# Kernel optimization log

Hardware: AMD Instinct MI355X
Metric: run time of the kernel (lower is better)

The kernel has to match this reference:

```python
import jax, jax.numpy as jnp
import numpy as np

N_NODES = 50000
N_EDGES = 500000
N_GRAPHS = 64
IN_DIM = 6
FFM_DIM = 128
GNN_DIM = 1024
OUT_DIM = 256
SCALES = (1.0, 5.0, 10.0, 30.0)
EPS = 1e-5


def setup_inputs() -> dict:
    key = jax.random.key(0)
    ks = jax.random.split(key, 16)
    x = jax.random.normal(ks[0], (N_NODES, IN_DIM), dtype=jnp.float32)
    edge_index = jax.random.randint(ks[1], (2, N_EDGES), 0, N_NODES, dtype=jnp.int32)
    node_coords = jax.random.normal(ks[2], (N_NODES, 3), dtype=jnp.float32)
    batch = jnp.sort(jax.random.randint(ks[3], (N_NODES,), 0, N_GRAPHS, dtype=jnp.int32))
    s6 = 1.0 / np.sqrt(IN_DIM)
    sg = 1.0 / np.sqrt(GNN_DIM)
    cat_dim = GNN_DIM + len(SCALES) * 2 * FFM_DIM
    sc = 1.0 / np.sqrt(cat_dim)
    return {
        "x": x, "edge_index": edge_index, "node_coords": node_coords, "batch": batch,
        "B": jax.random.normal(ks[4], (3, FFM_DIM), dtype=jnp.float32),
        "W1_l": jax.random.uniform(ks[5], (IN_DIM, GNN_DIM), jnp.float32, -s6, s6),
        "b1": jnp.zeros((GNN_DIM,), jnp.float32),
        "W1_r": jax.random.uniform(ks[6], (IN_DIM, GNN_DIM), jnp.float32, -s6, s6),
        "g1": jnp.ones((GNN_DIM,), jnp.float32), "be1": jnp.zeros((GNN_DIM,), jnp.float32),
        "W2_l": jax.random.uniform(ks[7], (GNN_DIM, GNN_DIM), jnp.float32, -sg, sg),
        "b2": jnp.zeros((GNN_DIM,), jnp.float32),
        "W2_r": jax.random.uniform(ks[8], (GNN_DIM, GNN_DIM), jnp.float32, -sg, sg),
        "g2": jnp.ones((GNN_DIM,), jnp.float32), "be2": jnp.zeros((GNN_DIM,), jnp.float32),
        "Wfc": jax.random.uniform(ks[9], (cat_dim, OUT_DIM), jnp.float32, -sc, sc),
        "bfc": jnp.zeros((OUT_DIM,), jnp.float32),
        "gfc": jnp.ones((OUT_DIM,), jnp.float32), "befc": jnp.zeros((OUT_DIM,), jnp.float32),
    }


def layer_norm(h, g, b):
    mu = jnp.mean(h, axis=-1, keepdims=True)
    var = jnp.mean(jnp.square(h - mu), axis=-1, keepdims=True)
    return (h - mu) * jax.lax.rsqrt(var + EPS) * g + b


def sage_conv(h, src, dst, Wl, bl, Wr):
    # mean aggregation of source features at destination nodes (PyG SAGEConv)
    agg = jax.ops.segment_sum(h[src], dst, num_segments=N_NODES)
    cnt = jax.ops.segment_sum(jnp.ones((src.shape[0],), h.dtype), dst, num_segments=N_NODES)
    agg = agg / jnp.maximum(cnt, 1.0)[:, None]
    return agg @ Wl + bl + h @ Wr


def reference(x, edge_index, node_coords, batch, B, W1_l, b1, W1_r, g1, be1,
              W2_l, b2, W2_r, g2, be2, Wfc, bfc, gfc, befc):
    src, dst = edge_index[0], edge_index[1]
    h = jax.nn.relu(layer_norm(sage_conv(x, src, dst, W1_l, b1, W1_r), g1, be1))
    h = jax.nn.relu(layer_norm(sage_conv(h, src, dst, W2_l, b2, W2_r), g2, be2))
    # multi-scale Fourier features on coordinates
    feats = []
    for s in SCALES:
        proj = (node_coords * s) @ B
        feats.append(jnp.sin(proj))
        feats.append(jnp.cos(proj))
    h_cat = jnp.concatenate([h] + feats, axis=1)
    # global mean pool per graph
    sums = jax.ops.segment_sum(h_cat, batch, num_segments=N_GRAPHS)
    cnts = jax.ops.segment_sum(jnp.ones((N_NODES,), h_cat.dtype), batch, num_segments=N_GRAPHS)
    h_g = sums / jnp.maximum(cnts, 1.0)[:, None]
    return layer_norm(h_g @ Wfc + bfc, gfc, befc)
```

## Files before the change

kernel.cpp:

```cpp
#include <hip/hip_runtime.h>
#include <hip/hip_bf16.h>


#define N_NODES 50000
#define N_EDGES 500000
#define N_GRAPHS 64
#define IN_DIM 6
#define GNN_DIM 1024
#define OUT_DIM 256
#define CAT_DIM 2048
#define M_PAD 50176

typedef __attribute__((ext_vector_type(8))) short short8;
typedef __attribute__((ext_vector_type(4))) float f32x4;

__device__ int g_cnt[N_NODES + 1];
__device__ int g_cursor[N_NODES];
__device__ int g_gcnt[N_GRAPHS];
__device__ int g_rowptr[N_NODES + 1];
__device__ int g_goff[N_GRAPHS + 1];
__device__ int g_esrc[N_EDGES];
__device__ __attribute__((aligned(256))) unsigned short g_w2lt[(size_t)GNN_DIM * GNN_DIM];
__device__ __attribute__((aligned(256))) unsigned short g_w2rt[(size_t)GNN_DIM * GNN_DIM];
__device__ float g_agg1[(size_t)N_NODES * IN_DIM];
__device__ __attribute__((aligned(256))) unsigned short g_h[(size_t)M_PAD * GNN_DIM];
__device__ __attribute__((aligned(256))) unsigned short g_agg2[(size_t)M_PAD * GNN_DIM];
__device__ __attribute__((aligned(256))) unsigned short g_h2[(size_t)M_PAD * GNN_DIM];
__device__ float g_gpool[(size_t)N_GRAPHS * CAT_DIM];

__device__ __forceinline__ float bflo(int u) { return __uint_as_float(((unsigned)u) << 16); }
__device__ __forceinline__ float bfhi(int u) { return __uint_as_float(((unsigned)u) & 0xffff0000u); }
__device__ __forceinline__ unsigned short f2bf(float f) {
    unsigned u = __float_as_uint(f);
    unsigned rounded = u + 0x7fff + ((u >> 16) & 1);
    return (unsigned short)(rounded >> 16);
}
__device__ __forceinline__ int pack2(unsigned short a, unsigned short b) {
    return (int)((unsigned)a | ((unsigned)b << 16));
}

__global__ void zero_kernel() {
    int i = blockIdx.x * 256 + threadIdx.x;
    if (i <= N_NODES) g_cnt[i] = 0;
    if (i < N_NODES) g_cursor[i] = 0;
    if (i < N_GRAPHS) g_gcnt[i] = 0;
    if (i < N_GRAPHS * CAT_DIM) g_gpool[i] = 0.f;
}

__global__ void count_kernel(const int* __restrict__ dst, const int* __restrict__ batch) {
    int i = blockIdx.x * 256 + threadIdx.x;
    if (i < N_EDGES) atomicAdd(&g_cnt[dst[i]], 1);
    if (i < N_NODES) atomicAdd(&g_gcnt[batch[i]], 1);
}

__global__ __launch_bounds__(1024) void scan_kernel() {
    const int CH = 49;
    int t = threadIdx.x;
    int base = t * CH;
    int s = 0;
    #pragma unroll
    for (int i = 0; i < CH; ++i) {
        int n = base + i;
        s += (n < N_NODES) ? g_cnt[n] : 0;
    }
    int lane = t & 63, w = t >> 6;
    int x = s;
    #pragma unroll
    for (int off = 1; off < 64; off <<= 1) {
        int y = __shfl_up(x, off);
        if (lane >= off) x += y;
    }
    __shared__ int wsum[16], woff[16];
    if (lane == 63) wsum[w] = x;
    __syncthreads();
    if (t == 0) { int a = 0; for (int i = 0; i < 16; ++i) { woff[i] = a; a += wsum[i]; } }
    __syncthreads();
    int excl = x - s + woff[w];
    #pragma unroll
    for (int i = 0; i < CH; ++i) {
        int n = base + i;
        if (n <= N_NODES) g_rowptr[n] = excl;
        if (n < N_NODES) excl += g_cnt[n];
    }
    if (t < 64) {
        int v = g_gcnt[t];
        int xx = v;
        #pragma unroll
        for (int off = 1; off < 64; off <<= 1) {
            int y = __shfl_up(xx, off);
            if ((t & 63) >= off) xx += y;
        }
        g_goff[t + 1] = xx;
        if (t == 0) g_goff[0] = 0;
    }
}

__global__ void scatter_kernel(const int* __restrict__ src, const int* __restrict__ dst) {
    int e = blockIdx.x * 256 + threadIdx.x;
    if (e >= N_EDGES) return;
    int d = dst[e];
    int pos = atomicAdd(&g_cursor[d], 1);
    g_esrc[g_rowptr[d] + pos] = src[e];
}

__global__ void transpose_bf16(const float* __restrict__ WA, const float* __restrict__ WB,
                               unsigned short* __restrict__ TA, unsigned short* __restrict__ TB) {
    __shared__ float tile[32][33];
    int id = blockIdx.x & 1023;
    const float* W = (blockIdx.x >> 10) ? WB : WA;
    unsigned short* Wt = (blockIdx.x >> 10) ? TB : TA;
    int bx = id & 31, by = id >> 5;
    int tx = threadIdx.x & 31, ty = threadIdx.x >> 5;
    for (int i = 0; i < 32; i += 8)
        tile[ty + i][tx] = W[(size_t)(by * 32 + ty + i) * GNN_DIM + bx * 32 + tx];
    __syncthreads();
    for (int i = 0; i < 32; i += 8)
        Wt[(size_t)(bx * 32 + ty + i) * GNN_DIM + by * 32 + tx] = f2bf(tile[tx][ty + i]);
}

__global__ void l1_agg_kernel(const float* __restrict__ x) {
    int id = blockIdx.x * 256 + threadIdx.x;
    int n = id >> 3, slot = id & 7;
    if (n >= N_NODES || slot >= IN_DIM) return;
    int beg = g_rowptr[n], end = g_rowptr[n + 1];
    float s = 0.f;
    for (int i = beg; i < end; ++i) s += x[(size_t)g_esrc[i] * IN_DIM + slot];
    g_agg1[n * IN_DIM + slot] = s / (float)max(end - beg, 1);
}

__global__ __launch_bounds__(256) void l1_transform_kernel(
        const float* __restrict__ x,
        const float* __restrict__ W1l, const float* __restrict__ b1,
        const float* __restrict__ W1r, const float* __restrict__ g1,
        const float* __restrict__ be1) {
    int t = threadIdx.x;
    int nb = blockIdx.x * 8;
    float4 wl[6], wr[6];
    #pragma unroll
    for (int k = 0; k < 6; ++k) {
        wl[k] = *(const float4*)&W1l[k * GNN_DIM + t * 4];
        wr[k] = *(const float4*)&W1r[k * GNN_DIM + t * 4];
    }
    float4 bb = *(const float4*)&b1[t * 4];
    float4 gg = *(const float4*)&g1[t * 4];
    float4 be = *(const float4*)&be1[t * 4];
    __shared__ float sx[48], sa[48];
    if (t < 48) sx[t] = x[nb * 6 + t];
    else if (t < 96) sa[t - 48] = g_agg1[nb * 6 + (t - 48)];
    __syncthreads();
    __shared__ float s1[4], s2[4];
    for (int u = 0; u < 8; ++u) {
        int n = nb + u;
        float4 v = bb;
        #pragma unroll
        for (int k = 0; k < 6; ++k) {
            float a = sa[u * 6 + k], xx = sx[u * 6 + k];
            v.x += a * wl[k].x + xx * wr[k].x;
            v.y += a * wl[k].y + xx * wr[k].y;
            v.z += a * wl[k].z + xx * wr[k].z;
            v.w += a * wl[k].w + xx * wr[k].w;
        }
        float sum = v.x + v.y + v.z + v.w;
        float sq  = v.x*v.x + v.y*v.y + v.z*v.z + v.w*v.w;
        #pragma unroll
        for (int off = 32; off; off >>= 1) { sum += __shfl_xor(sum, off); sq += __shfl_xor(sq, off); }
        if ((t & 63) == 0) { s1[t >> 6] = sum; s2[t >> 6] = sq; }
        __syncthreads();
        sum = s1[0] + s1[1] + s1[2] + s1[3];
        sq  = s2[0] + s2[1] + s2[2] + s2[3];
        __syncthreads();
        float mu = sum * (1.f / GNN_DIM);
        float var = sq * (1.f / GNN_DIM) - mu * mu;
        float rstd = rsqrtf(var + 1e-5f);
        float y0 = fmaxf((v.x - mu) * rstd * gg.x + be.x, 0.f);
        float y1 = fmaxf((v.y - mu) * rstd * gg.y + be.y, 0.f);
        float y2 = fmaxf((v.z - mu) * rstd * gg.z + be.z, 0.f);
        float y3 = fmaxf((v.w - mu) * rstd * gg.w + be.w, 0.f);
        int2 pk;
        pk.x = pack2(f2bf(y0), f2bf(y1));
        pk.y = pack2(f2bf(y2), f2bf(y3));
        *(int2*)(g_h + (size_t)n * GNN_DIM + t * 4) = pk;
    }
}

__global__ __launch_bounds__(256) void l2_agg_kernel() {
    int w = threadIdx.x >> 6, lane = threadIdx.x & 63;
    int n = blockIdx.x * 4 + w;
    int beg = g_rowptr[n], end = g_rowptr[n + 1];
    float s[16];
    #pragma unroll
    for (int j = 0; j < 16; ++j) s[j] = 0.f;
    const int4* hp = (const int4*)g_h;
    for (int i = beg; i < end; i += 8) {
        int idx[8]; float msk[8]; int4 va[8], vb[8];
        #pragma unroll
        for (int j = 0; j < 8; ++j) {
            int e = i + j;
            int cl = (e < end) ? e : beg;
            idx[j] = g_esrc[cl];
            msk[j] = (e < end) ? 1.f : 0.f;
        }
        #pragma unroll
        for (int j = 0; j < 8; ++j) {
            va[j] = hp[(size_t)idx[j] * 128 + lane];
            vb[j] = hp[(size_t)idx[j] * 128 + 64 + lane];
        }
        #pragma unroll
        for (int j = 0; j < 8; ++j) {
            float m = msk[j];
            s[0]  += m * bflo(va[j].x); s[1]  += m * bfhi(va[j].x);
            s[2]  += m * bflo(va[j].y); s[3]  += m * bfhi(va[j].y);
            s[4]  += m * bflo(va[j].z); s[5]  += m * bfhi(va[j].z);
            s[6]  += m * bflo(va[j].w); s[7]  += m * bfhi(va[j].w);
            s[8]  += m * bflo(vb[j].x); s[9]  += m * bfhi(vb[j].x);
            s[10] += m * bflo(vb[j].y); s[11] += m * bfhi(vb[j].y);
            s[12] += m * bflo(vb[j].z); s[13] += m * bfhi(vb[j].z);
            s[14] += m * bflo(vb[j].w); s[15] += m * bfhi(vb[j].w);
        }
    }
    float inv = 1.f / (float)max(end - beg, 1);
    int4 o0, o1;
    o0.x = pack2(f2bf(s[0] * inv),  f2bf(s[1] * inv));
    o0.y = pack2(f2bf(s[2] * inv),  f2bf(s[3] * inv));
    o0.z = pack2(f2bf(s[4] * inv),  f2bf(s[5] * inv));
    o0.w = pack2(f2bf(s[6] * inv),  f2bf(s[7] * inv));
    o1.x = pack2(f2bf(s[8] * inv),  f2bf(s[9] * inv));
    o1.y = pack2(f2bf(s[10] * inv), f2bf(s[11] * inv));
    o1.z = pack2(f2bf(s[12] * inv), f2bf(s[13] * inv));
    o1.w = pack2(f2bf(s[14] * inv), f2bf(s[15] * inv));
    *(int4*)(g_agg2 + (size_t)n * GNN_DIM + (size_t)lane * 8) = o0;
    *(int4*)(g_agg2 + (size_t)n * GNN_DIM + 512 + (size_t)lane * 8) = o1;
}

#define BM 128
#define BN 128
#define BK 64

__global__ __launch_bounds__(256) void gemm2_kernel(const float* __restrict__ bias) {
    __shared__ __attribute__((aligned(16))) unsigned short As[BM * BK];
    __shared__ __attribute__((aligned(16))) unsigned short Bs[BN * BK];
    int i = blockIdx.x;
    int xcd = i & 7;
    int j = i >> 3;
    int bm = xcd * 49 + (j >> 3);
    int bn = j & 7;
    int row0 = bm * BM, col0 = bn * BN;
    int t = threadIdx.x;
    int lane = t & 63, wid = t >> 6;
    int wr = wid >> 1, wc = wid & 1;
    f32x4 acc[4][4] = {};
    int c0 = t;
    for (int seg = 0; seg < 2; ++seg) {
        const unsigned short* A  = seg ? g_h : g_agg2;
        const unsigned short* Bt = seg ? g_w2rt : g_w2lt;
        for (int k0 = 0; k0 < GNN_DIM; k0 += BK) {
            __syncthreads();
            #pragma unroll
            for (int u = 0; u < 4; ++u) {
                int c = c0 + u * 256;
                int r = c >> 3;
                int kb = (c & 7) * 16;
                int kbs = kb ^ ((r & 7) << 4);
                __builtin_amdgcn_global_load_lds(
                    (const __attribute__((address_space(1))) void*)(A + (size_t)(row0 + r) * GNN_DIM + k0 + (kbs >> 1)),
                    (__attribute__((address_space(3))) void*)(As + c * 8), 16, 0, 0);
            }
            #pragma unroll
            for (int u = 0; u < 4; ++u) {
                int c = c0 + u * 256;
                int r = c >> 3;
                int kb = (c & 7) * 16;
                int kbs = kb ^ ((r & 7) << 4);
                __builtin_amdgcn_global_load_lds(
                    (const __attribute__((address_space(1))) void*)(Bt + (size_t)(col0 + r) * GNN_DIM + k0 + (kbs >> 1)),
                    (__attribute__((address_space(3))) void*)(Bs + c * 8), 16, 0, 0);
            }
            asm volatile("s_waitcnt vmcnt(0)" ::: "memory");
            __syncthreads();
            #pragma unroll
            for (int kk = 0; kk < BK; kk += 32) {
                short8 a[4], b[4];
                int krd = kk + (lane >> 4) * 8;
                #pragma unroll
                for (int m = 0; m < 4; ++m) {
                    int row = wr * 64 + m * 16 + (lane & 15);
                    int ks = ((krd * 2) ^ ((row & 7) << 4)) >> 1;
                    a[m] = *(const short8*)&As[row * BK + ks];
                }
                #pragma unroll
                for (int n = 0; n < 4; ++n) {
                    int row = wc * 64 + n * 16 + (lane & 15);
                    int ks = ((krd * 2) ^ ((row & 7) << 4)) >> 1;
                    b[n] = *(const short8*)&Bs[row * BK + ks];
                }
                #pragma unroll
                for (int m = 0; m < 4; ++m)
                    #pragma unroll
                    for (int n = 0; n < 4; ++n)
                        acc[m][n] = __builtin_amdgcn_mfma_f32_16x16x32_bf16(a[m], b[n], acc[m][n], 0, 0, 0);
            }
        }
    }
    #pragma unroll
    for (int m = 0; m < 4; ++m) {
        #pragma unroll
        for (int n = 0; n < 4; ++n) {
            int col = col0 + wc * 64 + n * 16 + (lane & 15);
            int rbase = row0 + wr * 64 + m * 16 + (lane >> 4) * 4;
            float bv = bias[col];
            #pragma unroll
            for (int r = 0; r < 4; ++r) {
                float v = acc[m][n][r] + bv;
                g_h2[(size_t)(rbase + r) * GNN_DIM + col] = f2bf(v);
            }
        }
    }
}

__global__ __launch_bounds__(256) void pool_h_kernel(const float* __restrict__ g2,
                                                     const float* __restrict__ be2) {
    int g = blockIdx.x >> 3, sl = blockIdx.x & 7;
    int t = threadIdx.x;
    int beg = g_goff[g], end = g_goff[g + 1];
    int cnt = end - beg;
    int per = (cnt + 7) >> 3;
    int s0 = beg + sl * per, s1v = min(s0 + per, end);
    if (s0 >= s1v) return;
    float4 gg = *(const float4*)&g2[t * 4];
    float4 be = *(const float4*)&be2[t * 4];
    __shared__ float r1[4], r2[4];
    float a0 = 0.f, a1 = 0.f, a2 = 0.f, a3 = 0.f;
    int2 wv = *(const int2*)(g_h2 + (size_t)s0 * GNN_DIM + t * 4);
    for (int n = s0; n < s1v; ++n) {
        int2 w = wv;
        if (n + 1 < s1v) wv = *(const int2*)(g_h2 + (size_t)(n + 1) * GNN_DIM + t * 4);
        float v0 = bflo(w.x), v1 = bfhi(w.x), v2 = bflo(w.y), v3 = bfhi(w.y);
        float sum = v0 + v1 + v2 + v3;
        float sq  = v0*v0 + v1*v1 + v2*v2 + v3*v3;
        #pragma unroll
        for (int off = 32; off; off >>= 1) { sum += __shfl_xor(sum, off); sq += __shfl_xor(sq, off); }
        if ((t & 63) == 0) { r1[t >> 6] = sum; r2[t >> 6] = sq; }
        __syncthreads();
        sum = r1[0] + r1[1] + r1[2] + r1[3];
        sq  = r2[0] + r2[1] + r2[2] + r2[3];
        __syncthreads();
        float mu = sum * (1.f / GNN_DIM);
        float var = sq * (1.f / GNN_DIM) - mu * mu;
        float rstd = rsqrtf(var + 1e-5f);
        a0 += fmaxf((v0 - mu) * rstd * gg.x + be.x, 0.f);
        a1 += fmaxf((v1 - mu) * rstd * gg.y + be.y, 0.f);
        a2 += fmaxf((v2 - mu) * rstd * gg.z + be.z, 0.f);
        a3 += fmaxf((v3 - mu) * rstd * gg.w + be.w, 0.f);
    }
    atomicAdd(&g_gpool[g * CAT_DIM + t * 4 + 0], a0);
    atomicAdd(&g_gpool[g * CAT_DIM + t * 4 + 1], a1);
    atomicAdd(&g_gpool[g * CAT_DIM + t * 4 + 2], a2);
    atomicAdd(&g_gpool[g * CAT_DIM + t * 4 + 3], a3);
}

__global__ __launch_bounds__(256) void pool_f_kernel(const float* __restrict__ coords,
                                                     const float* __restrict__ Bmat) {
    int g = blockIdx.x >> 2, sl = blockIdx.x & 3;
    int t = threadIdx.x;
    int beg = g_goff[g], end = g_goff[g + 1];
    int cnt = end - beg;
    int per = (cnt + 3) >> 2;
    int s0 = beg + sl * per, s1 = min(s0 + per, end);
    const float SC[4] = {1.f, 5.f, 10.f, 30.f};
    int si0 = t >> 7, c0 = t & 127;
    int si1 = si0 + 2;
    float b00 = Bmat[c0] * SC[si0], b01 = Bmat[128 + c0] * SC[si0], b02 = Bmat[256 + c0] * SC[si0];
    float b10 = Bmat[c0] * SC[si1], b11 = Bmat[128 + c0] * SC[si1], b12 = Bmat[256 + c0] * SC[si1];
    float ss0 = 0.f, cs0 = 0.f, ss1 = 0.f, cs1 = 0.f;
    __shared__ float sc[256 * 3];
    for (int base = s0; base < s1; base += 256) {
        int m = min(256, s1 - base);
        __syncthreads();
        for (int q = t; q < 3 * m; q += 256) sc[q] = coords[base * 3 + q];
        __syncthreads();
        for (int i = 0; i < m; ++i) {
            float x0 = sc[i * 3], y0 = sc[i * 3 + 1], z0 = sc[i * 3 + 2];
            float p0 = x0 * b00 + y0 * b01 + z0 * b02;
            float p1 = x0 * b10 + y0 * b11 + z0 * b12;
            ss0 += __sinf(p0); cs0 += __cosf(p0);
            ss1 += __sinf(p1); cs1 += __cosf(p1);
        }
    }
    if (s0 < s1) {
        float* gp = g_gpool + g * CAT_DIM + GNN_DIM;
        atomicAdd(&gp[si0 * 256 + c0], ss0);
        atomicAdd(&gp[si0 * 256 + 128 + c0], cs0);
        atomicAdd(&gp[si1 * 256 + c0], ss1);
        atomicAdd(&gp[si1 * 256 + 128 + c0], cs1);
    }
}

__global__ __launch_bounds__(256) void final_kernel(
        const float* __restrict__ Wfc, const float* __restrict__ bfc,
        const float* __restrict__ gfc, const float* __restrict__ befc,
        float* __restrict__ out) {
    int g = blockIdx.x, t = threadIdx.x;
    int beg = g_goff[g], end = g_goff[g + 1];
    float inv = 1.f / (float)max(end - beg, 1);
    __shared__ float hg[CAT_DIM];
    for (int i = t; i < CAT_DIM; i += 256) hg[i] = g_gpool[g * CAT_DIM + i] * inv;
    __syncthreads();
    float acc = bfc[t];
    for (int k = 0; k < CAT_DIM; ++k) acc = fmaf(hg[k], Wfc[(size_t)k * OUT_DIM + t], acc);
    float sum = acc, sq = acc * acc;
    #pragma unroll
    for (int off = 32; off; off >>= 1) { sum += __shfl_xor(sum, off); sq += __shfl_xor(sq, off); }
    __shared__ float s1[4], s2[4];
    if ((t & 63) == 0) { s1[t >> 6] = sum; s2[t >> 6] = sq; }
    __syncthreads();
    sum = s1[0] + s1[1] + s1[2] + s1[3];
    sq  = s2[0] + s2[1] + s2[2] + s2[3];
    float mu = sum * (1.f / OUT_DIM);
    float var = sq * (1.f / OUT_DIM) - mu * mu;
    float rstd = rsqrtf(var + 1e-5f);
    out[g * OUT_DIM + t] = (acc - mu) * rstd * gfc[t] + befc[t];
}

extern "C" void kernel_launch(void* const* d_in, const int* in_sizes, int n_in,
                              void* d_out, int out_size, void* d_ws, size_t ws_size,
                              hipStream_t stream) {
    const float* x      = (const float*)d_in[0];
    const int*   ei     = (const int*)d_in[1];
    const float* coords = (const float*)d_in[2];
    const int*   batch  = (const int*)d_in[3];
    const float* Bmat   = (const float*)d_in[4];
    const float* W1l    = (const float*)d_in[5];
    const float* b1     = (const float*)d_in[6];
    const float* W1r    = (const float*)d_in[7];
    const float* g1     = (const float*)d_in[8];
    const float* be1    = (const float*)d_in[9];
    const float* W2l    = (const float*)d_in[10];
    const float* b2     = (const float*)d_in[11];
    const float* W2r    = (const float*)d_in[12];
    const float* g2     = (const float*)d_in[13];
    const float* be2    = (const float*)d_in[14];
    const float* Wfc    = (const float*)d_in[15];
    const float* bfc    = (const float*)d_in[16];
    const float* gfc    = (const float*)d_in[17];
    const float* befc   = (const float*)d_in[18];
    const int* src = ei;
    const int* dst = ei + N_EDGES;
    float* out = (float*)d_out;
    (void)in_sizes; (void)n_in; (void)out_size; (void)d_ws; (void)ws_size;

    unsigned short* w2lt;  hipGetSymbolAddress((void**)&w2lt, HIP_SYMBOL(g_w2lt));
    unsigned short* w2rt;  hipGetSymbolAddress((void**)&w2rt, HIP_SYMBOL(g_w2rt));

    zero_kernel<<<512, 256, 0, stream>>>();
    count_kernel<<<(N_EDGES + 255) / 256, 256, 0, stream>>>(dst, batch);
    scan_kernel<<<1, 1024, 0, stream>>>();
    scatter_kernel<<<(N_EDGES + 255) / 256, 256, 0, stream>>>(src, dst);

    transpose_bf16<<<2048, 256, 0, stream>>>(W2l, W2r, w2lt, w2rt);

    l1_agg_kernel<<<(N_NODES * 8 + 255) / 256, 256, 0, stream>>>(x);
    l1_transform_kernel<<<N_NODES / 8, 256, 0, stream>>>(x, W1l, b1, W1r, g1, be1);

    l2_agg_kernel<<<N_NODES / 4, 256, 0, stream>>>();

    gemm2_kernel<<<(M_PAD / BM) * (GNN_DIM / BN), 256, 0, stream>>>(b2);

    pool_h_kernel<<<N_GRAPHS * 8, 256, 0, stream>>>(g2, be2);
    pool_f_kernel<<<N_GRAPHS * 4, 256, 0, stream>>>(coords, Bmat);

    final_kernel<<<N_GRAPHS, 256, 0, stream>>>(Wfc, bfc, gfc, befc, out);
}
```

Baseline: 885.9 us.

## Gather layer-2 neighbor features from an FP8 copy and restructure pooling per wave

```diff
diff --git a/kernel.cpp b/kernel.cpp
--- a/kernel.cpp
+++ b/kernel.cpp
@@ -13,6 +13,12 @@
 
 typedef __attribute__((ext_vector_type(8))) short short8;
 typedef __attribute__((ext_vector_type(4))) float f32x4;
+
+#if defined(__has_builtin)
+#if __has_builtin(__builtin_amdgcn_cvt_pk_fp8_f32) && __has_builtin(__builtin_amdgcn_cvt_pk_f32_fp8)
+#define HW_FP8 1
+#endif
+#endif
 
 __device__ int g_cnt[N_NODES + 1];
 __device__ int g_cursor[N_NODES];
@@ -24,6 +30,7 @@
 __device__ __attribute__((aligned(256))) unsigned short g_w2rt[(size_t)GNN_DIM * GNN_DIM];
 __device__ float g_agg1[(size_t)N_NODES * IN_DIM];
 __device__ __attribute__((aligned(256))) unsigned short g_h[(size_t)M_PAD * GNN_DIM];
+__device__ __attribute__((aligned(256))) unsigned g_h8w[(size_t)M_PAD * (GNN_DIM / 4)];
 __device__ __attribute__((aligned(256))) unsigned short g_agg2[(size_t)M_PAD * GNN_DIM];
 __device__ __attribute__((aligned(256))) unsigned short g_h2[(size_t)M_PAD * GNN_DIM];
 __device__ float g_gpool[(size_t)N_GRAPHS * CAT_DIM];
@@ -38,6 +45,22 @@
 __device__ __forceinline__ int pack2(unsigned short a, unsigned short b) {
     return (int)((unsigned)a | ((unsigned)b << 16));
 }
+
+#ifndef HW_FP8
+__device__ __forceinline__ unsigned enc8(float f) {
+    if (!(f >= 0.015625f)) return 0;
+    if (f > 448.f) f = 448.f;
+    unsigned u = __float_as_uint(f);
+    u += 0x7FFFF + ((u >> 20) & 1);
+    unsigned e = (u >> 23) & 0xFF;
+    return ((e - 120) << 3) | ((u >> 20) & 7);
+}
+__device__ __forceinline__ float dec8(unsigned b) {
+    unsigned e = (b >> 3) & 15, m = b & 7;
+    unsigned f = ((e + 120) << 23) | (m << 20);
+    return e ? __uint_as_float(f) : 0.f;
+}
+#endif
 
 __global__ void zero_kernel() {
     int i = blockIdx.x * 256 + threadIdx.x;
@@ -180,8 +203,28 @@
         pk.x = pack2(f2bf(y0), f2bf(y1));
         pk.y = pack2(f2bf(y2), f2bf(y3));
         *(int2*)(g_h + (size_t)n * GNN_DIM + t * 4) = pk;
-    }
-}
+#ifdef HW_FP8
+        int p8 = __builtin_amdgcn_cvt_pk_fp8_f32(y0, y1, 0, false);
+        p8 = __builtin_amdgcn_cvt_pk_fp8_f32(y2, y3, p8, true);
+        g_h8w[(size_t)n * 256 + t] = (unsigned)p8;
+#else
+        g_h8w[(size_t)n * 256 + t] =
+            enc8(y0) | (enc8(y1) << 8) | (enc8(y2) << 16) | (enc8(y3) << 24);
+#endif
+    }
+}
+
+#ifdef HW_FP8
+#define DEC_ACC(word, b) do { \
+    auto p0_ = __builtin_amdgcn_cvt_pk_f32_fp8((int)(word), false); \
+    auto p1_ = __builtin_amdgcn_cvt_pk_f32_fp8((int)(word), true);  \
+    s[(b)+0] += m * p0_[0]; s[(b)+1] += m * p0_[1]; \
+    s[(b)+2] += m * p1_[0]; s[(b)+3] += m * p1_[1]; } while (0)
+#else
+#define DEC_ACC(word, b) do { unsigned w_ = (unsigned)(word); \
+    s[(b)+0] += m * dec8(w_ & 255);        s[(b)+1] += m * dec8((w_ >> 8) & 255); \
+    s[(b)+2] += m * dec8((w_ >> 16) & 255); s[(b)+3] += m * dec8(w_ >> 24); } while (0)
+#endif
 
 __global__ __launch_bounds__(256) void l2_agg_kernel() {
     int w = threadIdx.x >> 6, lane = threadIdx.x & 63;
@@ -190,9 +233,9 @@
     float s[16];
     #pragma unroll
     for (int j = 0; j < 16; ++j) s[j] = 0.f;
-    const int4* hp = (const int4*)g_h;
+    const int4* hp = (const int4*)g_h8w;
     for (int i = beg; i < end; i += 8) {
-        int idx[8]; float msk[8]; int4 va[8], vb[8];
+        int idx[8]; float msk[8]; int4 v[8];
         #pragma unroll
         for (int j = 0; j < 8; ++j) {
             int e = i + j;
@@ -201,21 +244,12 @@
             msk[j] = (e < end) ? 1.f : 0.f;
         }
         #pragma unroll
-        for (int j = 0; j < 8; ++j) {
-            va[j] = hp[(size_t)idx[j] * 128 + lane];
-            vb[j] = hp[(size_t)idx[j] * 128 + 64 + lane];
-        }
+        for (int j = 0; j < 8; ++j) v[j] = hp[(size_t)idx[j] * 64 + lane];
         #pragma unroll
         for (int j = 0; j < 8; ++j) {
             float m = msk[j];
-            s[0]  += m * bflo(va[j].x); s[1]  += m * bfhi(va[j].x);
-            s[2]  += m * bflo(va[j].y); s[3]  += m * bfhi(va[j].y);
-            s[4]  += m * bflo(va[j].z); s[5]  += m * bfhi(va[j].z);
-            s[6]  += m * bflo(va[j].w); s[7]  += m * bfhi(va[j].w);
-            s[8]  += m * bflo(vb[j].x); s[9]  += m * bfhi(vb[j].x);
-            s[10] += m * bflo(vb[j].y); s[11] += m * bfhi(vb[j].y);
-            s[12] += m * bflo(vb[j].z); s[13] += m * bfhi(vb[j].z);
-            s[14] += m * bflo(vb[j].w); s[15] += m * bfhi(vb[j].w);
+            DEC_ACC(v[j].x, 0); DEC_ACC(v[j].y, 4);
+            DEC_ACC(v[j].z, 8); DEC_ACC(v[j].w, 12);
         }
     }
     float inv = 1.f / (float)max(end - beg, 1);
@@ -228,8 +262,8 @@
     o1.y = pack2(f2bf(s[10] * inv), f2bf(s[11] * inv));
     o1.z = pack2(f2bf(s[12] * inv), f2bf(s[13] * inv));
     o1.w = pack2(f2bf(s[14] * inv), f2bf(s[15] * inv));
-    *(int4*)(g_agg2 + (size_t)n * GNN_DIM + (size_t)lane * 8) = o0;
-    *(int4*)(g_agg2 + (size_t)n * GNN_DIM + 512 + (size_t)lane * 8) = o1;
+    *(int4*)(g_agg2 + (size_t)n * GNN_DIM + (size_t)lane * 16) = o0;
+    *(int4*)(g_agg2 + (size_t)n * GNN_DIM + (size_t)lane * 16 + 8) = o1;
 }
 
 #define BM 128
@@ -321,41 +355,57 @@
                                                      const float* __restrict__ be2) {
     int g = blockIdx.x >> 3, sl = blockIdx.x & 7;
     int t = threadIdx.x;
+    int w = t >> 6, lane = t & 63;
     int beg = g_goff[g], end = g_goff[g + 1];
     int cnt = end - beg;
     int per = (cnt + 7) >> 3;
     int s0 = beg + sl * per, s1v = min(s0 + per, end);
-    if (s0 >= s1v) return;
-    float4 gg = *(const float4*)&g2[t * 4];
-    float4 be = *(const float4*)&be2[t * 4];
-    __shared__ float r1[4], r2[4];
-    float a0 = 0.f, a1 = 0.f, a2 = 0.f, a3 = 0.f;
-    int2 wv = *(const int2*)(g_h2 + (size_t)s0 * GNN_DIM + t * 4);
-    for (int n = s0; n < s1v; ++n) {
-        int2 w = wv;
-        if (n + 1 < s1v) wv = *(const int2*)(g_h2 + (size_t)(n + 1) * GNN_DIM + t * 4);
-        float v0 = bflo(w.x), v1 = bfhi(w.x), v2 = bflo(w.y), v3 = bfhi(w.y);
-        float sum = v0 + v1 + v2 + v3;
-        float sq  = v0*v0 + v1*v1 + v2*v2 + v3*v3;
+    float gA[8], bA[8], gB[8], bB[8];
+    #pragma unroll
+    for (int j = 0; j < 8; ++j) {
+        gA[j] = g2[8 * lane + j];        bA[j] = be2[8 * lane + j];
+        gB[j] = g2[512 + 8 * lane + j];  bB[j] = be2[512 + 8 * lane + j];
+    }
+    float aA[8], aB[8];
+    #pragma unroll
+    for (int j = 0; j < 8; ++j) { aA[j] = 0.f; aB[j] = 0.f; }
+    for (int n = s0 + w; n < s1v; n += 4) {
+        const int4* rp = (const int4*)(g_h2 + (size_t)n * GNN_DIM);
+        int4 w0 = rp[lane], w1 = rp[64 + lane];
+        float vA[8] = { bflo(w0.x), bfhi(w0.x), bflo(w0.y), bfhi(w0.y),
+                        bflo(w0.z), bfhi(w0.z), bflo(w0.w), bfhi(w0.w) };
+        float vB[8] = { bflo(w1.x), bfhi(w1.x), bflo(w1.y), bfhi(w1.y),
+                        bflo(w1.z), bfhi(w1.z), bflo(w1.w), bfhi(w1.w) };
+        float sum = 0.f, sq = 0.f;
+        #pragma unroll
+        for (int j = 0; j < 8; ++j) {
+            sum += vA[j] + vB[j];
+            sq  += vA[j] * vA[j] + vB[j] * vB[j];
+        }
         #pragma unroll
         for (int off = 32; off; off >>= 1) { sum += __shfl_xor(sum, off); sq += __shfl_xor(sq, off); }
-        if ((t & 63) == 0) { r1[t >> 6] = sum; r2[t >> 6] = sq; }
-        __syncthreads();
-        sum = r1[0] + r1[1] + r1[2] + r1[3];
-        sq  = r2[0] + r2[1] + r2[2] + r2[3];
-        __syncthreads();
         float mu = sum * (1.f / GNN_DIM);
         float var = sq * (1.f / GNN_DIM) - mu * mu;
         float rstd = rsqrtf(var + 1e-5f);
-        a0 += fmaxf((v0 - mu) * rstd * gg.x + be.x, 0.f);
-        a1 += fmaxf((v1 - mu) * rstd * gg.y + be.y, 0.f);
-        a2 += fmaxf((v2 - mu) * rstd * gg.z + be.z, 0.f);
-        a3 += fmaxf((v3 - mu) * rstd * gg.w + be.w, 0.f);
-    }
-    atomicAdd(&g_gpool[g * CAT_DIM + t * 4 + 0], a0);
-    atomicAdd(&g_gpool[g * CAT_DIM + t * 4 + 1], a1);
-    atomicAdd(&g_gpool[g * CAT_DIM + t * 4 + 2], a2);
-    atomicAdd(&g_gpool[g * CAT_DIM + t * 4 + 3], a3);
+        #pragma unroll
+        for (int j = 0; j < 8; ++j) {
+            aA[j] += fmaxf((vA[j] - mu) * rstd * gA[j] + bA[j], 0.f);
+            aB[j] += fmaxf((vB[j] - mu) * rstd * gB[j] + bB[j], 0.f);
+        }
+    }
+    __shared__ float lacc[4][GNN_DIM];
+    #pragma unroll
+    for (int j = 0; j < 8; ++j) {
+        lacc[w][8 * lane + j] = aA[j];
+        lacc[w][512 + 8 * lane + j] = aB[j];
+    }
+    __syncthreads();
+    #pragma unroll
+    for (int q = 0; q < 4; ++q) {
+        int d = t * 4 + q;
+        float r = lacc[0][d] + lacc[1][d] + lacc[2][d] + lacc[3][d];
+        atomicAdd(&g_gpool[g * CAT_DIM + d], r);
+    }
 }
 
 __global__ __launch_bounds__(256) void pool_f_kernel(const float* __restrict__ coords,
```

New measurement: 800.7 us. 9.6% less time.
